# Performance work log

Measured on AMD Instinct MI355X. Metric: run time of the kernel, lower is better.

Reference implementation:

```python
import jax, jax.numpy as jnp
import numpy as np
from jax import lax

B, P, S, H, F, V, O = 32, 24, 48, 512, 64, 50000, 16
EPS = 1e-5


def _lstm_scan(inputs, Wih, Whh, b):
    # inputs: [T, B, D]; PyTorch gate order i, f, g, o
    def step(carry, xt):
        h, c = carry
        g = xt @ Wih.T + h @ Whh.T + b
        i, f, gg, o = jnp.split(g, 4, axis=-1)
        c = jax.nn.sigmoid(f) * c + jax.nn.sigmoid(i) * jnp.tanh(gg)
        h = jax.nn.sigmoid(o) * jnp.tanh(c)
        return (h, c), h
    b_ = inputs.shape[1]
    h0 = jnp.zeros((b_, Whh.shape[1]), inputs.dtype)
    _, hs = lax.scan(step, (h0, h0), inputs)
    return hs


def setup_inputs() -> dict:
    key = jax.random.key(0)
    ks = jax.random.split(key, 16)
    x = jax.random.randint(ks[0], (B, P, S), 0, V)
    lens = jnp.sort(jax.random.randint(ks[1], (B,), 1, P + 1))[::-1]
    lens = lens.at[0].set(P)  # pack_padded: sorted desc, max len == P
    tok_len = jax.random.randint(ks[2], (B, P), 1, S + 1)
    tok_len = tok_len * (jnp.arange(P)[None, :] < lens[:, None])
    x_mask = jnp.arange(S)[None, None, :] >= tok_len[:, :, None]  # True = pad
    x_feature = jax.random.normal(ks[3], (B, P, S, F), dtype=jnp.float32)
    emb = jax.random.normal(ks[4], (V, H), dtype=jnp.float32) * 0.02
    w_attn = jax.random.normal(ks[5], (H,), dtype=jnp.float32) * 0.02
    b_attn = jnp.zeros((), jnp.float32)
    D = H + F
    s = 1.0 / np.sqrt(H)
    u = lambda k, sh: jax.random.uniform(k, sh, jnp.float32, -s, s)
    Wih_f, Whh_f = u(ks[6], (4 * H, D)), u(ks[7], (4 * H, H))
    bih_f, bhh_f = u(ks[8], (4 * H,)), u(ks[9], (4 * H,))
    Wih_b, Whh_b = u(ks[10], (4 * H, D)), u(ks[11], (4 * H, H))
    bih_b, bhh_b = u(ks[12], (4 * H,)), u(ks[13], (4 * H,))
    Wfc = u(ks[14], (O, 2 * H))
    bfc = jnp.zeros((O,), jnp.float32)
    gamma = jnp.ones((O,), jnp.float32)
    beta = jnp.zeros((O,), jnp.float32)
    return {"x": x, "x_mask": x_mask, "x_feature": x_feature,
            "sentences_len": lens, "clause": 0, "cls": 0,
            "emb": emb, "w_attn": w_attn, "b_attn": b_attn,
            "Wih_f": Wih_f, "Whh_f": Whh_f, "bih_f": bih_f, "bhh_f": bhh_f,
            "Wih_b": Wih_b, "Whh_b": Whh_b, "bih_b": bih_b, "bhh_b": bhh_b,
            "Wfc": Wfc, "bfc": bfc, "gamma": gamma, "beta": beta}


def reference(x, x_mask, x_feature, sentences_len, clause, cls,
              emb, w_attn, b_attn,
              Wih_f, Whh_f, bih_f, bhh_f,
              Wih_b, Whh_b, bih_b, bhh_b,
              Wfc, bfc, gamma, beta):
    # --- per-sentence embed + linear self-attention + masked sum pooling ---
    e = emb[x]                                             # [B,P,S,H]
    scores = jnp.einsum('bpsh,h->bps', e, w_attn) + b_attn  # [B,P,S]
    scores = jnp.where(x_mask, -1e30, scores)
    alpha = jax.nn.softmax(scores, axis=-1)
    alpha = jnp.where(x_mask, 0.0, alpha)                  # zeros empty sents; relu(softmax)=softmax
    valid = (~x_mask).astype(e.dtype)
    weighted = e * alpha[..., None]
    cat = jnp.concatenate([weighted, x_feature], axis=-1) * valid[..., None]
    rep = cat.sum(axis=2)                                  # [B,P,H+F]
    seq = jnp.transpose(rep, (1, 0, 2))                    # time-major [P,B,H+F]

    # --- packed bidirectional LSTM (per-sequence reversal for bwd dir) ---
    t = jnp.arange(P)[:, None]                             # [P,1]
    lens = sentences_len[None, :]                          # [1,B]
    valid_t = (t < lens)                                   # [P,B]
    h_fwd = _lstm_scan(seq, Wih_f, Whh_f, bih_f + bhh_f)
    rev_idx = jnp.clip(lens - 1 - t, 0)                    # [P,B]
    rev_in = jnp.take_along_axis(seq, rev_idx[..., None], axis=0)
    h_bwd_rev = _lstm_scan(rev_in, Wih_b, Whh_b, bih_b + bhh_b)
    h_bwd = jnp.take_along_axis(h_bwd_rev, rev_idx[..., None], axis=0)
    out_seq = jnp.concatenate([h_fwd, h_bwd], axis=-1) * valid_t[..., None]  # pad_packed zeros

    # --- tail: last timestep, fc, train-mode BN, relu, log_softmax(dim=0) ---
    last = out_seq[-1]                                     # [B,2H]
    z = jnp.reshape(last.T, (B, 2 * H))                    # faithful transpose+view quirk
    y = z @ Wfc.T + bfc                                    # [B,O]
    mean = y.mean(axis=0)
    var = y.var(axis=0)                                    # biased, as torch BN normalization
    y = gamma * (y - mean) / jnp.sqrt(var + EPS) + beta
    y = jax.nn.relu(y)
    return jax.nn.log_softmax(y, axis=0)
```

## Files before the change

### kernel.cpp

```cpp
#include <hip/hip_runtime.h>
#include <math.h>

#define BB_ 32
#define PP_ 24
#define SS_ 48
#define HH_ 512
#define FF_ 64
#define DD_ 576
#define G4_ 2048

typedef __attribute__((ext_vector_type(8))) short short8;
typedef __attribute__((ext_vector_type(4))) float f32x4;

__device__ __forceinline__ float sigf(float x) { return 1.f / (1.f + expf(-x)); }

__device__ __forceinline__ unsigned short f2bf(float f) {
    unsigned int u = __float_as_uint(f);
    u += 0x7FFFu + ((u >> 16) & 1u);
    return (unsigned short)(u >> 16);
}

__global__ void __launch_bounds__(256) prep_kernel(
        const float* __restrict__ Whh, unsigned short* __restrict__ Bf,
        const float* __restrict__ Wih, unsigned short* __restrict__ Wbf,
        float* __restrict__ AfA,
        const unsigned int* __restrict__ maskw, int* __restrict__ mode,
        int* __restrict__ flags)
{
    int blk = blockIdx.x, tid = threadIdx.x;
    if (blk < 512) {
        int idx = blk * 256 + tid;
        int lane = idx & 63;
        int ks = (idx >> 6) & 15;
        int ti = (idx >> 10) & 1;
        int nb = idx >> 11;
        int c = lane & 15, q = lane >> 4;
        int nrow = (ti * 2 + (c >> 3)) * HH_ + nb * 8 + (c & 7);
        int k0 = ks * 32 + q * 8;
        const float* src = Whh + (size_t)nrow * HH_ + k0;
        unsigned int w0 = (unsigned int)f2bf(src[0]) | ((unsigned int)f2bf(src[1]) << 16);
        unsigned int w1 = (unsigned int)f2bf(src[2]) | ((unsigned int)f2bf(src[3]) << 16);
        unsigned int w2 = (unsigned int)f2bf(src[4]) | ((unsigned int)f2bf(src[5]) << 16);
        unsigned int w3 = (unsigned int)f2bf(src[6]) | ((unsigned int)f2bf(src[7]) << 16);
        *(uint4*)(Bf + (size_t)idx * 8) = make_uint4(w0, w1, w2, w3);
    } else if (blk < 1664) {
        int i = (blk - 512) * 256 + tid;
        float4 v = ((const float4*)Wih)[i];
        ushort4 o;
        o.x = f2bf(v.x); o.y = f2bf(v.y); o.z = f2bf(v.z); o.w = f2bf(v.w);
        ((ushort4*)Wbf)[i] = o;
    } else if (blk < 1728) {
        int idx = (blk - 1664) * 256 + tid;
        if (idx < 8192) AfA[idx] = 0.f;
    } else {
        __shared__ int s_u8, s_f32;
        if (tid == 0) { s_u8 = 0; s_f32 = 0; }
        __syncthreads();
        int u8 = 0, f32 = 0;
        for (int i = tid; i < 9216; i += 256) {
            unsigned int w = maskw[i];
            if (w == 0x3F800000u) f32 = 1;
            else if (w > 1u) u8 = 1;
        }
        if (u8) s_u8 = 1;
        if (f32) s_f32 = 1;
        if (tid < 64) flags[tid] = 0;
        __syncthreads();
        if (tid == 0) *mode = s_f32 ? 2 : (s_u8 ? 1 : 0);
    }
}

__global__ void attn_rep_kernel(const int* __restrict__ x,
                                const void* __restrict__ x_mask,
                                const int* __restrict__ mode_p,
                                const float* __restrict__ x_feature,
                                const float* __restrict__ emb,
                                const float* __restrict__ w_attn,
                                const float* __restrict__ b_attn,
                                float* __restrict__ seq)
{
    int bp = blockIdx.x;
    int b = bp / PP_, p = bp % PP_;
    int tid = threadIdx.x;
    __shared__ float wattn_s[HH_];
    __shared__ float sc_s[SS_];
    __shared__ float alpha_s[SS_];
    __shared__ int idx_s[SS_];
    __shared__ unsigned char msk_s[SS_];
    int mode = *mode_p;
    wattn_s[tid] = w_attn[tid];
    wattn_s[tid + 256] = w_attn[tid + 256];
    if (tid < SS_) {
        size_t i = (size_t)bp * SS_ + tid;
        idx_s[tid] = x[i];
        unsigned char mv;
        if (mode == 1)      mv = ((const unsigned char*)x_mask)[i];
        else if (mode == 2) mv = (((const float*)x_mask)[i] != 0.f);
        else                mv = (((const int*)x_mask)[i] != 0);
        msk_s[tid] = mv;
    }
    __syncthreads();
    int wave = tid >> 6, lane = tid & 63;
    for (int s = wave; s < SS_; s += 4) {
        const float* er = emb + (size_t)idx_s[s] * HH_;
        float acc = 0.f;
        #pragma unroll
        for (int j = 0; j < 8; ++j) {
            int d = lane * 8 + j;
            acc += er[d] * wattn_s[d];
        }
        #pragma unroll
        for (int off = 32; off > 0; off >>= 1) acc += __shfl_down(acc, off, 64);
        if (lane == 0) sc_s[s] = acc + b_attn[0];
    }
    __syncthreads();
    if (tid == 0) {
        float m = -3.4e38f;
        for (int s = 0; s < SS_; ++s) if (!msk_s[s] && sc_s[s] > m) m = sc_s[s];
        float sum = 0.f;
        for (int s = 0; s < SS_; ++s) {
            float a = 0.f;
            if (!msk_s[s]) { a = expf(sc_s[s] - m); sum += a; }
            alpha_s[s] = a;
        }
        float inv = (sum > 0.f) ? (1.f / sum) : 0.f;
        for (int s = 0; s < SS_; ++s) alpha_s[s] *= inv;
    }
    __syncthreads();
    float acc0 = 0.f, acc1 = 0.f;
    #pragma unroll 6
    for (int s = 0; s < SS_; ++s) {
        float a = alpha_s[s];
        const float* er = emb + (size_t)idx_s[s] * HH_;
        acc0 += a * er[tid];
        acc1 += a * er[tid + 256];
    }
    float* orow = seq + ((size_t)p * BB_ + b) * DD_;
    orow[tid] = acc0;
    orow[tid + 256] = acc1;
    if (tid < FF_) {
        float acc2 = 0.f;
        for (int s = 0; s < SS_; ++s)
            if (!msk_s[s]) acc2 += x_feature[((size_t)bp * SS_ + s) * FF_ + tid];
        orow[HH_ + tid] = acc2;
    }
}

__global__ void __launch_bounds__(256) in_gates_mfma_kernel(
        const float* __restrict__ A,
        const unsigned short* __restrict__ Wbf,
        const float* __restrict__ bih,
        const float* __restrict__ bhh,
        float* __restrict__ Cout)
{
    int tid = threadIdx.x, lane = tid & 63, w = tid >> 6;
    int m0 = blockIdx.y * 16;
    int nb = blockIdx.x * 128 + w * 32;
    int c = lane & 15, q = lane >> 4;
    const float* Ap = A + (size_t)(m0 + c) * DD_ + q * 8;
    const unsigned short* Bp0 = Wbf + (size_t)(nb + c) * DD_ + q * 8;
    const unsigned short* Bp1 = Bp0 + 16 * DD_;
    f32x4 acc0 = {0.f, 0.f, 0.f, 0.f}, acc1 = {0.f, 0.f, 0.f, 0.f};
    for (int k = 0; k < DD_; k += 32) {
        float4 alo = *(const float4*)(Ap + k);
        float4 ahi = *(const float4*)(Ap + k + 4);
        short8 a;
        a[0] = (short)f2bf(alo.x); a[1] = (short)f2bf(alo.y);
        a[2] = (short)f2bf(alo.z); a[3] = (short)f2bf(alo.w);
        a[4] = (short)f2bf(ahi.x); a[5] = (short)f2bf(ahi.y);
        a[6] = (short)f2bf(ahi.z); a[7] = (short)f2bf(ahi.w);
        short8 b0 = *(const short8*)(Bp0 + k);
        short8 b1 = *(const short8*)(Bp1 + k);
        acc0 = __builtin_amdgcn_mfma_f32_16x16x32_bf16(a, b0, acc0, 0, 0, 0);
        acc1 = __builtin_amdgcn_mfma_f32_16x16x32_bf16(a, b1, acc1, 0, 0, 0);
    }
    #pragma unroll
    for (int r = 0; r < 4; ++r) {
        int m = m0 + q * 4 + r;
        int n0 = nb + c, n1 = nb + 16 + c;
        Cout[(size_t)m * G4_ + n0] = acc0[r] + bih[n0] + bhh[n0];
        Cout[(size_t)m * G4_ + n1] = acc1[r] + bih[n1] + bhh[n1];
    }
}

__global__ void __launch_bounds__(256) bwd_last2_kernel(const float* __restrict__ seq,
        const int* __restrict__ lens,
        const float* __restrict__ Wih_b,
        const float* __restrict__ bih_b,
        const float* __restrict__ bhh_b,
        float* __restrict__ hb)
{
    __shared__ float xsT[DD_ * 33];
    __shared__ int pl[BB_];
    int tid = threadIdx.x;
    if (tid < BB_) pl[tid] = lens[tid] - 1;
    __syncthreads();
    for (int idx = tid; idx < BB_ * DD_; idx += 256) {
        int b2 = idx / DD_;
        int k = idx - b2 * DD_;
        xsT[k * 33 + b2] = seq[((size_t)pl[b2] * BB_ + b2) * DD_ + k];
    }
    __syncthreads();
    int b = tid & 31, ul = tid >> 5;
    int u = blockIdx.x * 8 + ul;
    const float* wi = Wih_b + (size_t)u * DD_;
    const float* wg = Wih_b + (size_t)(2 * HH_ + u) * DD_;
    const float* wo = Wih_b + (size_t)(3 * HH_ + u) * DD_;
    float gi = 0.f, gg = 0.f, go = 0.f;
    #pragma unroll 4
    for (int k = 0; k < DD_; k += 4) {
        float4 w1 = *(const float4*)(wi + k);
        float4 w2 = *(const float4*)(wg + k);
        float4 w3 = *(const float4*)(wo + k);
        float x0 = xsT[(k + 0) * 33 + b];
        float x1 = xsT[(k + 1) * 33 + b];
        float x2 = xsT[(k + 2) * 33 + b];
        float x3 = xsT[(k + 3) * 33 + b];
        gi += w1.x * x0 + w1.y * x1 + w1.z * x2 + w1.w * x3;
        gg += w2.x * x0 + w2.y * x1 + w2.z * x2 + w2.w * x3;
        go += w3.x * x0 + w3.y * x1 + w3.z * x2 + w3.w * x3;
    }
    gi += bih_b[u] + bhh_b[u];
    gg += bih_b[2 * HH_ + u] + bhh_b[2 * HH_ + u];
    go += bih_b[3 * HH_ + u] + bhh_b[3 * HH_ + u];
    float cc = sigf(gi) * tanhf(gg);
    hb[(size_t)b * HH_ + u] = sigf(go) * tanhf(cc);
}

__global__ void __launch_bounds__(256) lstm_persist_kernel(
        unsigned short* __restrict__ AfA, unsigned short* __restrict__ AfB,
        float* __restrict__ hbuf, const float* __restrict__ Ain,
        const unsigned short* __restrict__ Bfrag, int* __restrict__ flags)
{
    __shared__ float gl[32 * 33];
    __shared__ unsigned short hstage[256];
    int tid = threadIdx.x, lane = tid & 63, wv = tid >> 6;
    int mt = wv & 1, ti = wv >> 1;
    int nb = blockIdx.x;
    const short8* Bp = (const short8*)Bfrag + (((size_t)nb * 2 + ti) * 16) * 64 + lane;
    short8 bfr[16];
    #pragma unroll
    for (int ks = 0; ks < 16; ++ks) bfr[ks] = Bp[ks * 64];
    int c = lane & 15, q = lane >> 4;
    int g = ti * 2 + (c >> 3), ul = c & 7;
    int b2 = tid >> 3, u2 = tid & 7;
    int ug = nb * 8 + u2;
    float creg = 0.f;
    for (int t = 0; t < PP_; ++t) {
        const unsigned short* Af = (t & 1) ? AfB : AfA;
        unsigned short* An       = (t & 1) ? AfA : AfB;
        const float* Ain_t = Ain + (size_t)t * BB_ * G4_;
        float ainv[4];
        #pragma unroll
        for (int r = 0; r < 4; ++r)
            ainv[r] = Ain_t[(size_t)(mt * 16 + q * 4 + r) * G4_ + g * HH_ + nb * 8 + ul];
        const unsigned long long* Ap64 =
            (const unsigned long long*)Af + ((size_t)(mt * 16) * 64 + lane) * 2;
        short8 a[16];
        #pragma unroll
        for (int ks = 0; ks < 16; ++ks) {
            unsigned long long lo = __hip_atomic_load(Ap64 + (size_t)ks * 128,
                    __ATOMIC_RELAXED, __HIP_MEMORY_SCOPE_AGENT);
            unsigned long long hi = __hip_atomic_load(Ap64 + (size_t)ks * 128 + 1,
                    __ATOMIC_RELAXED, __HIP_MEMORY_SCOPE_AGENT);
            union { unsigned long long u[2]; short8 s; } cv;
            cv.u[0] = lo; cv.u[1] = hi;
            a[ks] = cv.s;
        }
        f32x4 acc = {0.f, 0.f, 0.f, 0.f};
        #pragma unroll
        for (int ks = 0; ks < 16; ++ks)
            acc = __builtin_amdgcn_mfma_f32_16x16x32_bf16(a[ks], bfr[ks], acc, 0, 0, 0);
        #pragma unroll
        for (int r = 0; r < 4; ++r) {
            float v = acc[r] + ainv[r];
            v = (g == 2) ? tanhf(v) : sigf(v);
            gl[(g * 8 + ul) * 33 + (mt * 16 + q * 4 + r)] = v;
        }
        __syncthreads();
        float iv = gl[(0  + u2) * 33 + b2];
        float fv = gl[(8  + u2) * 33 + b2];
        float gv = gl[(16 + u2) * 33 + b2];
        float ov = gl[(24 + u2) * 33 + b2];
        creg = fv * creg + iv * gv;
        float h = ov * tanhf(creg);
        if (t == PP_ - 1) {
            hbuf[(size_t)b2 * HH_ + ug] = h;
        } else {
            hstage[tid] = f2bf(h);
            __syncthreads();
            if (tid < 64) {
                int b2s = tid >> 1, hf2 = tid & 1;
                const unsigned short* hp = &hstage[b2s * 8 + hf2 * 4];
                unsigned long long v = (unsigned long long)hp[0]
                                     | ((unsigned long long)hp[1] << 16)
                                     | ((unsigned long long)hp[2] << 32)
                                     | ((unsigned long long)hp[3] << 48);
                size_t ub = ((((size_t)(b2s >> 4)) * 16 + (nb >> 2)) * 64
                             + ((b2s & 15) + 16 * (nb & 3))) * 8 + hf2 * 4;
                __hip_atomic_store((unsigned long long*)(An + ub), v,
                                   __ATOMIC_RELAXED, __HIP_MEMORY_SCOPE_AGENT);
            }
            __syncthreads();
            if (tid == 0)
                __hip_atomic_store(&flags[nb], t + 1,
                                   __ATOMIC_RELAXED, __HIP_MEMORY_SCOPE_AGENT);
            if (tid < 64) {
                int target = t + 1;
                while (true) {
                    int v = __hip_atomic_load(&flags[tid],
                            __ATOMIC_RELAXED, __HIP_MEMORY_SCOPE_AGENT);
                    if (__all(v >= target)) break;
                    __builtin_amdgcn_s_sleep(2);
                }
            }
            __syncthreads();
        }
    }
}

__global__ void __launch_bounds__(1024) head_fused_kernel(
        const float* __restrict__ hf, const float* __restrict__ hbwd,
        const int* __restrict__ lens,
        const float* __restrict__ Wfc, const float* __restrict__ bfc,
        const float* __restrict__ gamma, const float* __restrict__ beta,
        float* __restrict__ out)
{
    __shared__ float tileL[32 * 1024];
    __shared__ float lmask[BB_];
    __shared__ float part[1024];
    __shared__ float ys[16][33];
    __shared__ float cstat[16];
    int tid = threadIdx.x;
    if (tid < BB_) lmask[tid] = (lens[tid] == PP_) ? 1.f : 0.f;
    __syncthreads();
    for (int j = tid; j < 32 * 1024; j += 1024) {
        int bb = j >> 10, col = j & 1023;
        float v = (col < HH_) ? hf[(size_t)bb * HH_ + col]
                              : hbwd[(size_t)bb * HH_ + col - HH_];
        tileL[j] = v * lmask[bb];
    }
    __syncthreads();
    int outi = tid & 511, half = tid >> 9;
    int i = outi >> 4, o = outi & 15;
    const float* wrow = Wfc + (size_t)o * 1024;
    float acc = 0.f;
    for (int q = 0; q < 32; ++q) {
        int j = i * 32 + q;
        #pragma unroll
        for (int bb2 = 0; bb2 < 16; ++bb2) {
            int bb = half * 16 + bb2;
            acc += tileL[bb * 1024 + j] * wrow[q * 32 + bb];
        }
    }
    part[tid] = acc;
    __syncthreads();
    if (tid < 512) ys[o][i] = part[tid] + part[tid + 512] + bfc[o];
    __syncthreads();
    if (tid < 16) {
        float mean = 0.f;
        for (int ii = 0; ii < 32; ++ii) mean += ys[tid][ii];
        mean *= (1.f / 32.f);
        float var = 0.f;
        for (int ii = 0; ii < 32; ++ii) { float d = ys[tid][ii] - mean; var += d * d; }
        var *= (1.f / 32.f);
        float inv = 1.f / sqrtf(var + 1e-5f);
        float gmm = gamma[tid], bt = beta[tid];
        float mx = -3.4e38f;
        for (int ii = 0; ii < 32; ++ii) {
            float v = gmm * (ys[tid][ii] - mean) * inv + bt;
            v = fmaxf(v, 0.f);
            ys[tid][ii] = v;
            mx = fmaxf(mx, v);
        }
        float s = 0.f;
        for (int ii = 0; ii < 32; ++ii) s += expf(ys[tid][ii] - mx);
        cstat[tid] = mx + logf(s);
    }
    __syncthreads();
    if (tid < 512) out[tid] = ys[o][i] - cstat[o];
}

extern "C" void kernel_launch(void* const* d_in, const int* in_sizes, int n_in,
                              void* d_out, int out_size, void* d_ws, size_t ws_size,
                              hipStream_t stream) {
    const int* x            = (const int*)d_in[0];
    const void* xm          = d_in[1];
    const float* x_feature  = (const float*)d_in[2];
    const int* lens         = (const int*)d_in[3];
    const float* emb    = (const float*)d_in[6];
    const float* w_attn = (const float*)d_in[7];
    const float* b_attn = (const float*)d_in[8];
    const float* Wih_f  = (const float*)d_in[9];
    const float* Whh_f  = (const float*)d_in[10];
    const float* bih_f  = (const float*)d_in[11];
    const float* bhh_f  = (const float*)d_in[12];
    const float* Wih_b  = (const float*)d_in[13];
    const float* bih_b  = (const float*)d_in[15];
    const float* bhh_b  = (const float*)d_in[16];
    const float* Wfc    = (const float*)d_in[17];
    const float* bfc    = (const float*)d_in[18];
    const float* gamma  = (const float*)d_in[19];
    const float* beta   = (const float*)d_in[20];

    float* ws    = (float*)d_ws;
    float* seq   = ws;
    float* Ain   = seq + (size_t)PP_ * BB_ * DD_;
    float* hb    = Ain + (size_t)PP_ * BB_ * G4_;
    float* hbuf  = hb + (size_t)BB_ * HH_;
    float* AfA   = hbuf + (size_t)BB_ * HH_;
    float* AfB   = AfA + 8192;
    float* Bfrag = AfB + 8192;
    float* Wbf   = Bfrag + 524288;
    int*  flags  = (int*)(Wbf + 589824);
    int*  mflag  = flags + 64;

    float* outp = (float*)d_out;

    prep_kernel<<<dim3(1729), dim3(256), 0, stream>>>(
        Whh_f, (unsigned short*)Bfrag, Wih_f, (unsigned short*)Wbf,
        AfA, (const unsigned int*)xm, mflag, flags);
    attn_rep_kernel<<<dim3(BB_ * PP_), dim3(256), 0, stream>>>(
        x, xm, mflag, x_feature, emb, w_attn, b_attn, seq);
    in_gates_mfma_kernel<<<dim3(16, 48), dim3(256), 0, stream>>>(
        seq, (const unsigned short*)Wbf, bih_f, bhh_f, Ain);
    bwd_last2_kernel<<<dim3(64), dim3(256), 0, stream>>>(
        seq, lens, Wih_b, bih_b, bhh_b, hb);
    lstm_persist_kernel<<<dim3(64), dim3(256), 0, stream>>>(
        (unsigned short*)AfA, (unsigned short*)AfB, hbuf, Ain,
        (const unsigned short*)Bfrag, flags);
    head_fused_kernel<<<dim3(1), dim3(1024), 0, stream>>>(
        hbuf, hb, lens, Wfc, bfc, gamma, beta, outp);
}
```

Before: 491.7 us.

## Merge attention into prep kernel and run backward gates beside forward LSTM

Folds the attention-pooling kernel into the prep kernel. Each attention block now redoes the mask-format detection itself, compacts the unmasked tokens and computes scores only for those, using float4 loads. The backward last-step gate computation now runs as extra blocks of the persistent forward LSTM kernel, so it overlaps the recurrence instead of taking its own launch. The LSTM MFMA chain is split into two accumulators and the spin-wait sleep is shortened. Together these remove two kernel launches and the idle time between them. The cost is that every attention block rescans the whole mask, and the forward recurrence now shares the GPU with the added backward blocks.

New measurement: 441.2 us. 1.11x faster.

```diff
diff --git a/kernel.cpp b/kernel.cpp
--- a/kernel.cpp
+++ b/kernel.cpp
@@ -20,16 +20,93 @@
     return (unsigned short)(u >> 16);
 }
 
-__global__ void __launch_bounds__(256) prep_kernel(
+__global__ void __launch_bounds__(256) prep_attn_kernel(
+        const int* __restrict__ x, const unsigned int* __restrict__ maskw,
+        const float* __restrict__ x_feature, const float* __restrict__ emb,
+        const float* __restrict__ w_attn, const float* __restrict__ b_attn,
         const float* __restrict__ Whh, unsigned short* __restrict__ Bf,
         const float* __restrict__ Wih, unsigned short* __restrict__ Wbf,
-        float* __restrict__ AfA,
-        const unsigned int* __restrict__ maskw, int* __restrict__ mode,
-        int* __restrict__ flags)
+        float* __restrict__ AfA, int* __restrict__ flags,
+        float* __restrict__ seq)
 {
     int blk = blockIdx.x, tid = threadIdx.x;
-    if (blk < 512) {
-        int idx = blk * 256 + tid;
+    if (blk < 768) {
+        __shared__ float sc_s[SS_], alpha_s[SS_];
+        __shared__ int vtok[SS_], vpos[SS_];
+        __shared__ int nv_s, s_u8, s_f32;
+        __shared__ int idx_s[SS_];
+        __shared__ unsigned char msk_s[SS_];
+        if (tid == 0) { s_u8 = 0; s_f32 = 0; }
+        __syncthreads();
+        int u8 = 0, f32 = 0;
+        for (int i = tid; i < 9216; i += 256) {
+            unsigned int w = maskw[i];
+            if (w == 0x3F800000u) f32 = 1;
+            else if (w > 1u) u8 = 1;
+        }
+        if (u8) s_u8 = 1;
+        if (f32) s_f32 = 1;
+        __syncthreads();
+        int mode = s_f32 ? 2 : (s_u8 ? 1 : 0);
+        int bp = blk, b = bp / PP_, p = bp % PP_;
+        if (tid < SS_) {
+            size_t i = (size_t)bp * SS_ + tid;
+            idx_s[tid] = x[i];
+            unsigned char mv;
+            if (mode == 1)      mv = ((const unsigned char*)maskw)[i];
+            else if (mode == 2) mv = (((const float*)maskw)[i] != 0.f);
+            else                mv = (((const int*)maskw)[i] != 0);
+            msk_s[tid] = mv;
+        }
+        __syncthreads();
+        if (tid == 0) {
+            int nv = 0;
+            for (int s = 0; s < SS_; ++s)
+                if (!msk_s[s]) { vtok[nv] = idx_s[s]; vpos[nv] = s; ++nv; }
+            nv_s = nv;
+        }
+        __syncthreads();
+        int nv = nv_s;
+        int wave = tid >> 6, lane = tid & 63;
+        float4 wa0 = ((const float4*)w_attn)[lane];
+        float4 wa1 = ((const float4*)w_attn)[64 + lane];
+        for (int j = wave; j < nv; j += 4) {
+            const float4* er4 = (const float4*)(emb + (size_t)vtok[j] * HH_);
+            float4 v0 = er4[lane], v1 = er4[64 + lane];
+            float acc = v0.x * wa0.x + v0.y * wa0.y + v0.z * wa0.z + v0.w * wa0.w
+                      + v1.x * wa1.x + v1.y * wa1.y + v1.z * wa1.z + v1.w * wa1.w;
+            #pragma unroll
+            for (int off = 32; off > 0; off >>= 1) acc += __shfl_down(acc, off, 64);
+            if (lane == 0) sc_s[j] = acc + b_attn[0];
+        }
+        __syncthreads();
+        if (tid == 0) {
+            float m = -3.4e38f;
+            for (int j = 0; j < nv; ++j) if (sc_s[j] > m) m = sc_s[j];
+            float sum = 0.f;
+            for (int j = 0; j < nv; ++j) { float a = expf(sc_s[j] - m); alpha_s[j] = a; sum += a; }
+            float inv = (nv > 0) ? (1.f / sum) : 0.f;
+            for (int j = 0; j < nv; ++j) alpha_s[j] *= inv;
+        }
+        __syncthreads();
+        float acc0 = 0.f, acc1 = 0.f;
+        for (int j = 0; j < nv; ++j) {
+            float a = alpha_s[j];
+            const float* er = emb + (size_t)vtok[j] * HH_;
+            acc0 += a * er[tid];
+            acc1 += a * er[tid + 256];
+        }
+        float* orow = seq + ((size_t)p * BB_ + b) * DD_;
+        orow[tid] = acc0;
+        orow[tid + 256] = acc1;
+        if (tid < FF_) {
+            float accF = 0.f;
+            for (int j = 0; j < nv; ++j)
+                accF += x_feature[((size_t)bp * SS_ + vpos[j]) * FF_ + tid];
+            orow[HH_ + tid] = accF;
+        }
+    } else if (blk < 1280) {
+        int idx = (blk - 768) * 256 + tid;
         int lane = idx & 63;
         int ks = (idx >> 6) & 15;
         int ti = (idx >> 10) & 1;
@@ -43,106 +120,17 @@
         unsigned int w2 = (unsigned int)f2bf(src[4]) | ((unsigned int)f2bf(src[5]) << 16);
         unsigned int w3 = (unsigned int)f2bf(src[6]) | ((unsigned int)f2bf(src[7]) << 16);
         *(uint4*)(Bf + (size_t)idx * 8) = make_uint4(w0, w1, w2, w3);
-    } else if (blk < 1664) {
-        int i = (blk - 512) * 256 + tid;
+    } else if (blk < 2432) {
+        int i = (blk - 1280) * 256 + tid;
         float4 v = ((const float4*)Wih)[i];
         ushort4 o;
         o.x = f2bf(v.x); o.y = f2bf(v.y); o.z = f2bf(v.z); o.w = f2bf(v.w);
         ((ushort4*)Wbf)[i] = o;
-    } else if (blk < 1728) {
-        int idx = (blk - 1664) * 256 + tid;
+    } else if (blk < 2464) {
+        int idx = (blk - 2432) * 256 + tid;
         if (idx < 8192) AfA[idx] = 0.f;
     } else {
-        __shared__ int s_u8, s_f32;
-        if (tid == 0) { s_u8 = 0; s_f32 = 0; }
-        __syncthreads();
-        int u8 = 0, f32 = 0;
-        for (int i = tid; i < 9216; i += 256) {
-            unsigned int w = maskw[i];
-            if (w == 0x3F800000u) f32 = 1;
-            else if (w > 1u) u8 = 1;
-        }
-        if (u8) s_u8 = 1;
-        if (f32) s_f32 = 1;
         if (tid < 64) flags[tid] = 0;
-        __syncthreads();
-        if (tid == 0) *mode = s_f32 ? 2 : (s_u8 ? 1 : 0);
-    }
-}
-
-__global__ void attn_rep_kernel(const int* __restrict__ x,
-                                const void* __restrict__ x_mask,
-                                const int* __restrict__ mode_p,
-                                const float* __restrict__ x_feature,
-                                const float* __restrict__ emb,
-                                const float* __restrict__ w_attn,
-                                const float* __restrict__ b_attn,
-                                float* __restrict__ seq)
-{
-    int bp = blockIdx.x;
-    int b = bp / PP_, p = bp % PP_;
-    int tid = threadIdx.x;
-    __shared__ float wattn_s[HH_];
-    __shared__ float sc_s[SS_];
-    __shared__ float alpha_s[SS_];
-    __shared__ int idx_s[SS_];
-    __shared__ unsigned char msk_s[SS_];
-    int mode = *mode_p;
-    wattn_s[tid] = w_attn[tid];
-    wattn_s[tid + 256] = w_attn[tid + 256];
-    if (tid < SS_) {
-        size_t i = (size_t)bp * SS_ + tid;
-        idx_s[tid] = x[i];
-        unsigned char mv;
-        if (mode == 1)      mv = ((const unsigned char*)x_mask)[i];
-        else if (mode == 2) mv = (((const float*)x_mask)[i] != 0.f);
-        else                mv = (((const int*)x_mask)[i] != 0);
-        msk_s[tid] = mv;
-    }
-    __syncthreads();
-    int wave = tid >> 6, lane = tid & 63;
-    for (int s = wave; s < SS_; s += 4) {
-        const float* er = emb + (size_t)idx_s[s] * HH_;
-        float acc = 0.f;
-        #pragma unroll
-        for (int j = 0; j < 8; ++j) {
-            int d = lane * 8 + j;
-            acc += er[d] * wattn_s[d];
-        }
-        #pragma unroll
-        for (int off = 32; off > 0; off >>= 1) acc += __shfl_down(acc, off, 64);
-        if (lane == 0) sc_s[s] = acc + b_attn[0];
-    }
-    __syncthreads();
-    if (tid == 0) {
-        float m = -3.4e38f;
-        for (int s = 0; s < SS_; ++s) if (!msk_s[s] && sc_s[s] > m) m = sc_s[s];
-        float sum = 0.f;
-        for (int s = 0; s < SS_; ++s) {
-            float a = 0.f;
-            if (!msk_s[s]) { a = expf(sc_s[s] - m); sum += a; }
-            alpha_s[s] = a;
-        }
-        float inv = (sum > 0.f) ? (1.f / sum) : 0.f;
-        for (int s = 0; s < SS_; ++s) alpha_s[s] *= inv;
-    }
-    __syncthreads();
-    float acc0 = 0.f, acc1 = 0.f;
-    #pragma unroll 6
-    for (int s = 0; s < SS_; ++s) {
-        float a = alpha_s[s];
-        const float* er = emb + (size_t)idx_s[s] * HH_;
-        acc0 += a * er[tid];
-        acc1 += a * er[tid + 256];
-    }
-    float* orow = seq + ((size_t)p * BB_ + b) * DD_;
-    orow[tid] = acc0;
-    orow[tid + 256] = acc1;
-    if (tid < FF_) {
-        float acc2 = 0.f;
-        for (int s = 0; s < SS_; ++s)
-            if (!msk_s[s]) acc2 += x_feature[((size_t)bp * SS_ + s) * FF_ + tid];
-        orow[HH_ + tid] = acc2;
     }
 }
 
@@ -183,139 +171,140 @@
     }
 }
 
-__global__ void __launch_bounds__(256) bwd_last2_kernel(const float* __restrict__ seq,
-        const int* __restrict__ lens,
-        const float* __restrict__ Wih_b,
-        const float* __restrict__ bih_b,
-        const float* __restrict__ bhh_b,
-        float* __restrict__ hb)
-{
-    __shared__ float xsT[DD_ * 33];
-    __shared__ int pl[BB_];
-    int tid = threadIdx.x;
-    if (tid < BB_) pl[tid] = lens[tid] - 1;
-    __syncthreads();
-    for (int idx = tid; idx < BB_ * DD_; idx += 256) {
-        int b2 = idx / DD_;
-        int k = idx - b2 * DD_;
-        xsT[k * 33 + b2] = seq[((size_t)pl[b2] * BB_ + b2) * DD_ + k];
-    }
-    __syncthreads();
-    int b = tid & 31, ul = tid >> 5;
-    int u = blockIdx.x * 8 + ul;
-    const float* wi = Wih_b + (size_t)u * DD_;
-    const float* wg = Wih_b + (size_t)(2 * HH_ + u) * DD_;
-    const float* wo = Wih_b + (size_t)(3 * HH_ + u) * DD_;
-    float gi = 0.f, gg = 0.f, go = 0.f;
-    #pragma unroll 4
-    for (int k = 0; k < DD_; k += 4) {
-        float4 w1 = *(const float4*)(wi + k);
-        float4 w2 = *(const float4*)(wg + k);
-        float4 w3 = *(const float4*)(wo + k);
-        float x0 = xsT[(k + 0) * 33 + b];
-        float x1 = xsT[(k + 1) * 33 + b];
-        float x2 = xsT[(k + 2) * 33 + b];
-        float x3 = xsT[(k + 3) * 33 + b];
-        gi += w1.x * x0 + w1.y * x1 + w1.z * x2 + w1.w * x3;
-        gg += w2.x * x0 + w2.y * x1 + w2.z * x2 + w2.w * x3;
-        go += w3.x * x0 + w3.y * x1 + w3.z * x2 + w3.w * x3;
-    }
-    gi += bih_b[u] + bhh_b[u];
-    gg += bih_b[2 * HH_ + u] + bhh_b[2 * HH_ + u];
-    go += bih_b[3 * HH_ + u] + bhh_b[3 * HH_ + u];
-    float cc = sigf(gi) * tanhf(gg);
-    hb[(size_t)b * HH_ + u] = sigf(go) * tanhf(cc);
-}
-
-__global__ void __launch_bounds__(256) lstm_persist_kernel(
+__global__ void __launch_bounds__(256) lstm_bwd_kernel(
         unsigned short* __restrict__ AfA, unsigned short* __restrict__ AfB,
         float* __restrict__ hbuf, const float* __restrict__ Ain,
-        const unsigned short* __restrict__ Bfrag, int* __restrict__ flags)
+        const unsigned short* __restrict__ Bfrag, int* __restrict__ flags,
+        const float* __restrict__ seq, const int* __restrict__ lens,
+        const float* __restrict__ Wih_b, const float* __restrict__ bih_b,
+        const float* __restrict__ bhh_b, float* __restrict__ hbw)
 {
-    __shared__ float gl[32 * 33];
-    __shared__ unsigned short hstage[256];
-    int tid = threadIdx.x, lane = tid & 63, wv = tid >> 6;
-    int mt = wv & 1, ti = wv >> 1;
-    int nb = blockIdx.x;
-    const short8* Bp = (const short8*)Bfrag + (((size_t)nb * 2 + ti) * 16) * 64 + lane;
-    short8 bfr[16];
-    #pragma unroll
-    for (int ks = 0; ks < 16; ++ks) bfr[ks] = Bp[ks * 64];
-    int c = lane & 15, q = lane >> 4;
-    int g = ti * 2 + (c >> 3), ul = c & 7;
-    int b2 = tid >> 3, u2 = tid & 7;
-    int ug = nb * 8 + u2;
-    float creg = 0.f;
-    for (int t = 0; t < PP_; ++t) {
-        const unsigned short* Af = (t & 1) ? AfB : AfA;
-        unsigned short* An       = (t & 1) ? AfA : AfB;
-        const float* Ain_t = Ain + (size_t)t * BB_ * G4_;
-        float ainv[4];
+    __shared__ float smem[19040];
+    int tid = threadIdx.x;
+    if (blockIdx.x < 64) {
+        float* gl = smem;
+        unsigned short* hstage = (unsigned short*)(smem + 1056);
+        int lane = tid & 63, wv = tid >> 6;
+        int mt = wv & 1, ti = wv >> 1;
+        int nb = blockIdx.x;
+        const short8* Bp = (const short8*)Bfrag + (((size_t)nb * 2 + ti) * 16) * 64 + lane;
+        short8 bfr[16];
         #pragma unroll
-        for (int r = 0; r < 4; ++r)
-            ainv[r] = Ain_t[(size_t)(mt * 16 + q * 4 + r) * G4_ + g * HH_ + nb * 8 + ul];
-        const unsigned long long* Ap64 =
-            (const unsigned long long*)Af + ((size_t)(mt * 16) * 64 + lane) * 2;
-        short8 a[16];
-        #pragma unroll
-        for (int ks = 0; ks < 16; ++ks) {
-            unsigned long long lo = __hip_atomic_load(Ap64 + (size_t)ks * 128,
-                    __ATOMIC_RELAXED, __HIP_MEMORY_SCOPE_AGENT);
-            unsigned long long hi = __hip_atomic_load(Ap64 + (size_t)ks * 128 + 1,
-                    __ATOMIC_RELAXED, __HIP_MEMORY_SCOPE_AGENT);
-            union { unsigned long long u[2]; short8 s; } cv;
-            cv.u[0] = lo; cv.u[1] = hi;
-            a[ks] = cv.s;
-        }
-        f32x4 acc = {0.f, 0.f, 0.f, 0.f};
-        #pragma unroll
-        for (int ks = 0; ks < 16; ++ks)
-            acc = __builtin_amdgcn_mfma_f32_16x16x32_bf16(a[ks], bfr[ks], acc, 0, 0, 0);
-        #pragma unroll
-        for (int r = 0; r < 4; ++r) {
-            float v = acc[r] + ainv[r];
-            v = (g == 2) ? tanhf(v) : sigf(v);
-            gl[(g * 8 + ul) * 33 + (mt * 16 + q * 4 + r)] = v;
-        }
-        __syncthreads();
-        float iv = gl[(0  + u2) * 33 + b2];
-        float fv = gl[(8  + u2) * 33 + b2];
-        float gv = gl[(16 + u2) * 33 + b2];
-        float ov = gl[(24 + u2) * 33 + b2];
-        creg = fv * creg + iv * gv;
-        float h = ov * tanhf(creg);
-        if (t == PP_ - 1) {
-            hbuf[(size_t)b2 * HH_ + ug] = h;
-        } else {
-            hstage[tid] = f2bf(h);
-            __syncthreads();
-            if (tid < 64) {
-                int b2s = tid >> 1, hf2 = tid & 1;
-                const unsigned short* hp = &hstage[b2s * 8 + hf2 * 4];
-                unsigned long long v = (unsigned long long)hp[0]
-                                     | ((unsigned long long)hp[1] << 16)
-                                     | ((unsigned long long)hp[2] << 32)
-                                     | ((unsigned long long)hp[3] << 48);
-                size_t ub = ((((size_t)(b2s >> 4)) * 16 + (nb >> 2)) * 64
-                             + ((b2s & 15) + 16 * (nb & 3))) * 8 + hf2 * 4;
-                __hip_atomic_store((unsigned long long*)(An + ub), v,
-                                   __ATOMIC_RELAXED, __HIP_MEMORY_SCOPE_AGENT);
+        for (int ks = 0; ks < 16; ++ks) bfr[ks] = Bp[ks * 64];
+        int c = lane & 15, q = lane >> 4;
+        int g = ti * 2 + (c >> 3), ul = c & 7;
+        int b2 = tid >> 3, u2 = tid & 7;
+        int ug = nb * 8 + u2;
+        float creg = 0.f;
+        for (int t = 0; t < PP_; ++t) {
+            const unsigned short* Af = (t & 1) ? AfB : AfA;
+            unsigned short* An       = (t & 1) ? AfA : AfB;
+            const float* Ain_t = Ain + (size_t)t * BB_ * G4_;
+            float ainv[4];
+            #pragma unroll
+            for (int r = 0; r < 4; ++r)
+                ainv[r] = Ain_t[(size_t)(mt * 16 + q * 4 + r) * G4_ + g * HH_ + nb * 8 + ul];
+            const unsigned long long* Ap64 =
+                (const unsigned long long*)Af + ((size_t)(mt * 16) * 64 + lane) * 2;
+            short8 a[16];
+            #pragma unroll
+            for (int ks = 0; ks < 16; ++ks) {
+                unsigned long long lo = __hip_atomic_load(Ap64 + (size_t)ks * 128,
+                        __ATOMIC_RELAXED, __HIP_MEMORY_SCOPE_AGENT);
+                unsigned long long hi = __hip_atomic_load(Ap64 + (size_t)ks * 128 + 1,
+                        __ATOMIC_RELAXED, __HIP_MEMORY_SCOPE_AGENT);
+                union { unsigned long long u[2]; short8 s; } cv;
+                cv.u[0] = lo; cv.u[1] = hi;
+                a[ks] = cv.s;
+            }
+            f32x4 acA = {0.f, 0.f, 0.f, 0.f}, acB = {0.f, 0.f, 0.f, 0.f};
+            #pragma unroll
+            for (int ks = 0; ks < 16; ks += 2) {
+                acA = __builtin_amdgcn_mfma_f32_16x16x32_bf16(a[ks],     bfr[ks],     acA, 0, 0, 0);
+                acB = __builtin_amdgcn_mfma_f32_16x16x32_bf16(a[ks + 1], bfr[ks + 1], acB, 0, 0, 0);
+            }
+            #pragma unroll
+            for (int r = 0; r < 4; ++r) {
+                float v = acA[r] + acB[r] + ainv[r];
+                v = (g == 2) ? tanhf(v) : sigf(v);
+                gl[(g * 8 + ul) * 33 + (mt * 16 + q * 4 + r)] = v;
             }
             __syncthreads();
-            if (tid == 0)
-                __hip_atomic_store(&flags[nb], t + 1,
-                                   __ATOMIC_RELAXED, __HIP_MEMORY_SCOPE_AGENT);
-            if (tid < 64) {
-                int target = t + 1;
-                while (true) {
-                    int v = __hip_atomic_load(&flags[tid],
-                            __ATOMIC_RELAXED, __HIP_MEMORY_SCOPE_AGENT);
-                    if (__all(v >= target)) break;
-                    __builtin_amdgcn_s_sleep(2);
+            float iv = gl[(0  + u2) * 33 + b2];
+            float fv = gl[(8  + u2) * 33 + b2];
+            float gv = gl[(16 + u2) * 33 + b2];
+            float ov = gl[(24 + u2) * 33 + b2];
+            creg = fv * creg + iv * gv;
+            float h = ov * tanhf(creg);
+            if (t == PP_ - 1) {
+                hbuf[(size_t)b2 * HH_ + ug] = h;
+            } else {
+                hstage[tid] = f2bf(h);
+                __syncthreads();
+                if (tid < 64) {
+                    int b2s = tid >> 1, hf2 = tid & 1;
+                    const unsigned short* hp = &hstage[b2s * 8 + hf2 * 4];
+                    unsigned long long v = (unsigned long long)hp[0]
+                                         | ((unsigned long long)hp[1] << 16)
+                                         | ((unsigned long long)hp[2] << 32)
+                                         | ((unsigned long long)hp[3] << 48);
+                    size_t ub = ((((size_t)(b2s >> 4)) * 16 + (nb >> 2)) * 64
+                                 + ((b2s & 15) + 16 * (nb & 3))) * 8 + hf2 * 4;
+                    __hip_atomic_store((unsigned long long*)(An + ub), v,
+                                       __ATOMIC_RELAXED, __HIP_MEMORY_SCOPE_AGENT);
                 }
+                __syncthreads();
+                if (tid == 0)
+                    __hip_atomic_store(&flags[nb], t + 1,
+                                       __ATOMIC_RELAXED, __HIP_MEMORY_SCOPE_AGENT);
+                if (tid < 64) {
+                    int target = t + 1;
+                    while (true) {
+                        int v = __hip_atomic_load(&flags[tid],
+                                __ATOMIC_RELAXED, __HIP_MEMORY_SCOPE_AGENT);
+                        if (__all(v >= target)) break;
+                        __builtin_amdgcn_s_sleep(1);
+                    }
+                }
+                __syncthreads();
             }
-            __syncthreads();
-        }
+        }
+    } else {
+        float* xsT = smem;
+        int* pl = (int*)(smem + 19008);
+        int blk2 = blockIdx.x - 64;
+        if (tid < BB_) pl[tid] = lens[tid] - 1;
+        __syncthreads();
+        for (int idx = tid; idx < BB_ * DD_; idx += 256) {
+            int b2 = idx / DD_;
+            int k = idx - b2 * DD_;
+            xsT[k * 33 + b2] = seq[((size_t)pl[b2] * BB_ + b2) * DD_ + k];
+        }
+        __syncthreads();
+        int b = tid & 31, ul = tid >> 5;
+        int u = blk2 * 8 + ul;
+        const float* wi = Wih_b + (size_t)u * DD_;
+        const float* wg = Wih_b + (size_t)(2 * HH_ + u) * DD_;
+        const float* wo = Wih_b + (size_t)(3 * HH_ + u) * DD_;
+        float gi = 0.f, gg = 0.f, go = 0.f;
+        #pragma unroll 4
+        for (int k = 0; k < DD_; k += 4) {
+            float4 w1 = *(const float4*)(wi + k);
+            float4 w2 = *(const float4*)(wg + k);
+            float4 w3 = *(const float4*)(wo + k);
+            float x0 = xsT[(k + 0) * 33 + b];
+            float x1 = xsT[(k + 1) * 33 + b];
+            float x2 = xsT[(k + 2) * 33 + b];
+            float x3 = xsT[(k + 3) * 33 + b];
+            gi += w1.x * x0 + w1.y * x1 + w1.z * x2 + w1.w * x3;
+            gg += w2.x * x0 + w2.y * x1 + w2.z * x2 + w2.w * x3;
+            go += w3.x * x0 + w3.y * x1 + w3.z * x2 + w3.w * x3;
+        }
+        gi += bih_b[u] + bhh_b[u];
+        gg += bih_b[2 * HH_ + u] + bhh_b[2 * HH_ + u];
+        go += bih_b[3 * HH_ + u] + bhh_b[3 * HH_ + u];
+        float cc = sigf(gi) * tanhf(gg);
+        hbw[(size_t)b * HH_ + u] = sigf(go) * tanhf(cc);
     }
 }
 
@@ -413,22 +402,19 @@
     float* Bfrag = AfB + 8192;
     float* Wbf   = Bfrag + 524288;
     int*  flags  = (int*)(Wbf + 589824);
-    int*  mflag  = flags + 64;
 
     float* outp = (float*)d_out;
 
-    prep_kernel<<<dim3(1729), dim3(256), 0, stream>>>(
+    prep_attn_kernel<<<dim3(2465), dim3(256), 0, stream>>>(
+        x, (const unsigned int*)xm, x_feature, emb, w_attn, b_attn,
         Whh_f, (unsigned short*)Bfrag, Wih_f, (unsigned short*)Wbf,
-        AfA, (const unsigned int*)xm, mflag, flags);
-    attn_rep_kernel<<<dim3(BB_ * PP_), dim3(256), 0, stream>>>(
-        x, xm, mflag, x_feature, emb, w_attn, b_attn, seq);
+        AfA, flags, seq);
     in_gates_mfma_kernel<<<dim3(16, 48), dim3(256), 0, stream>>>(
         seq, (const unsigned short*)Wbf, bih_f, bhh_f, Ain);
-    bwd_last2_kernel<<<dim3(64), dim3(256), 0, stream>>>(
+    lstm_bwd_kernel<<<dim3(128), dim3(256), 0, stream>>>(
+        (unsigned short*)AfA, (unsigned short*)AfB, hbuf, Ain,
+        (const unsigned short*)Bfrag, flags,
         seq, lens, Wih_b, bih_b, bhh_b, hb);
-    lstm_persist_kernel<<<dim3(64), dim3(256), 0, stream>>>(
-        (unsigned short*)AfA, (unsigned short*)AfB, hbuf, Ain,
-        (const unsigned short*)Bfrag, flags);
     head_fused_kernel<<<dim3(1), dim3(1024), 0, stream>>>(
         hbuf, hb, lens, Wfc, bfc, gamma, beta, outp);
 }
```
